# Performance work log

Hardware: AMD Instinct MI355X
Metric: run time of the kernel (lower is better)

## Reference

```python
import jax, jax.numpy as jnp
import numpy as np

B, N, M, K = 2, 50000, 50000, 16
C_IN, C_ADD, C_MID = 64, 3, 16


def setup_inputs() -> dict:
    key = jax.random.key(0)
    k1, k2, k3, k4 = jax.random.split(key, 4)
    return {
        "input_features": jax.random.normal(k1, (B, N, C_IN), dtype=jnp.float32),
        "neighbor_inds": jax.random.randint(k2, (B, M, K), 0, N, dtype=jnp.int64),
        "weightnet": jax.random.normal(k3, (B, M, K, C_MID), dtype=jnp.float32),
        "additional_features": jax.random.normal(k4, (B, M, K, C_ADD), dtype=jnp.float32),
    }


def reference(input_features, neighbor_inds, weightnet, additional_features):
    # Gather neighbor features: [B, M, K, C_in]
    gathered = jax.vmap(lambda feat, idx: feat[idx])(input_features, neighbor_inds)
    # Concatenate additional per-neighbor features: [B, M, K, C_in + C_add]
    cat = jnp.concatenate([gathered, additional_features], axis=-1)
    # Weighted reduce over neighbors: [B, M, C_total, C_mid]
    out = jnp.einsum("bmkc,bmkw->bmcw", cat, weightnet)
    b, m = out.shape[:2]
    return out.reshape(b, m, -1)
```

## Files before the change

kernel.cpp:

```cpp
#include <hip/hip_runtime.h>
#include <cstdint>
#include <cstddef>


namespace {
constexpr int B_   = 2;
constexpr int N_   = 50000;
constexpr int M_   = 50000;
constexpr int KNB  = 16;
constexpr int CIN  = 64;
constexpr int COUT = 67 * 16;
constexpr int PAIRS = B_ * M_;
constexpr int FELEMS = B_ * N_ * CIN;
}

typedef unsigned int u32;
typedef float  f32x4  __attribute__((ext_vector_type(4)));
typedef short  short8 __attribute__((ext_vector_type(8)));
typedef u32    u32x4  __attribute__((ext_vector_type(4)));
typedef u32    u32x2  __attribute__((ext_vector_type(2)));

struct IdxS   { int v[16]; };
struct StageT { unsigned short bg[4][8]; float ad[8]; float wf[8]; };
struct StageF { float bg[4][8]; float ad[8]; float wf[8]; };

static __device__ __forceinline__ short8 pack_bf8(const float* x) {
  u32x4 w;
  #pragma unroll
  for (int q = 0; q < 4; ++q)
    w[q] = __builtin_amdgcn_perm(__builtin_bit_cast(u32, x[2*q+1]),
                                 __builtin_bit_cast(u32, x[2*q]),
                                 0x07060302u);
  return __builtin_bit_cast(short8, w);
}

static __device__ __forceinline__ u32 bfrne(float x) {
  u32 u = __builtin_bit_cast(u32, x);
  return (u + 0x7FFFu + ((u >> 16) & 1u)) >> 16;
}

__global__ __launch_bounds__(256)
void cvt_feat_bf16(const float* __restrict__ src, unsigned short* __restrict__ dst) {
  const int n4 = FELEMS / 4;
  int i = blockIdx.x * blockDim.x + threadIdx.x;
  const int stride = gridDim.x * blockDim.x;
  const f32x4* s4 = reinterpret_cast<const f32x4*>(src);
  for (; i < n4; i += stride) {
    f32x4 v = s4[i];
    u32x2 w;
    w[0] = bfrne(v[0]) | (bfrne(v[1]) << 16);
    w[1] = bfrne(v[2]) | (bfrne(v[3]) << 16);
    *reinterpret_cast<u32x2*>(dst + 4 * (size_t)i) = w;
  }
}

static __device__ __forceinline__ void load_idx(const int* __restrict__ idxp, IdxS& r) {
  #pragma unroll
  for (int j = 0; j < 16; ++j)
    r.v[j] = __builtin_amdgcn_readfirstlane(idxp[j]);
}

static __device__ __forceinline__ void load_stage_t(const unsigned short* __restrict__ fb,
                                                    const float* __restrict__ wnp,
                                                    const float* __restrict__ adp,
                                                    const IdxS& I, int lane, StageT& S) {
  const int cc = lane & 15;
  if (lane < 32) {
    const int hi = lane >> 4;
    int rows[8];
    #pragma unroll
    for (int j = 0; j < 8; ++j) rows[j] = hi ? I.v[j + 8] : I.v[j];
    #pragma unroll
    for (int j = 0; j < 8; ++j) {
      const u32 rb = ((u32)rows[j]) << 6;
      #pragma unroll
      for (int t = 0; t < 4; ++t)
        S.bg[t][j] = fb[rb + (u32)(t * 16 + cc)];
    }
    const u32 woff = (hi ? 128u : 0u) + (u32)cc;
    #pragma unroll
    for (int j = 0; j < 8; ++j)
      S.wf[j] = __builtin_nontemporal_load(wnp + woff + j * 16);
    if (cc < 3) {
      const u32 aoff = (hi ? 24u : 0u) + (u32)cc;
      #pragma unroll
      for (int j = 0; j < 8; ++j)
        S.ad[j] = __builtin_nontemporal_load(adp + aoff + j * 3);
    }
  }
}

static __device__ __forceinline__ void compute_store_t(const StageT& S,
                                                       float* __restrict__ op, int lane) {
  const int cc = lane & 15, g = lane >> 4;
  const int soff = cc * 16 + g * 4;
  const short8 a = pack_bf8(S.wf);
  #pragma unroll
  for (int t = 0; t < 4; ++t) {
    short8 b;
    #pragma unroll
    for (int j = 0; j < 8; ++j) b[j] = (short)S.bg[t][j];
    f32x4 acc = {0.f, 0.f, 0.f, 0.f};
    acc = __builtin_amdgcn_mfma_f32_16x16x32_bf16(a, b, acc, 0, 0, 0);
    __builtin_nontemporal_store(acc, reinterpret_cast<f32x4*>(op + soff + t * 256));
  }
  {
    const short8 b = pack_bf8(S.ad);
    f32x4 acc = {0.f, 0.f, 0.f, 0.f};
    acc = __builtin_amdgcn_mfma_f32_16x16x32_bf16(a, b, acc, 0, 0, 0);
    if (cc < 3)
      __builtin_nontemporal_store(acc, reinterpret_cast<f32x4*>(op + soff + 1024));
  }
}

__global__ __launch_bounds__(256, 3)
void pconv6_tbl(const unsigned short* __restrict__ tbl, const int* __restrict__ inds,
                const float* __restrict__ wnet, const float* __restrict__ addf,
                float* __restrict__ out)
{
  const int lane = threadIdx.x & 63;
  const int gw = __builtin_amdgcn_readfirstlane(
      (int)((blockIdx.x * blockDim.x + threadIdx.x) >> 6));
  const int nw = (int)((gridDim.x * blockDim.x) >> 6);
  if (gw >= PAIRS) return;

  StageT sA = {}, sB = {};
  IdxS iA, iB;

  int p = gw;
  load_idx(inds + (size_t)p * KNB, iA);
  { const int p1 = (p + nw < PAIRS) ? (p + nw) : gw;
    load_idx(inds + (size_t)p1 * KNB, iB); }
  { const int b = p / M_;
    load_stage_t(tbl + (size_t)b * N_ * CIN, wnet + (size_t)p * 256,
                 addf + (size_t)p * 48, iA, lane, sA); }

  while (true) {
    {
      const int pf = (p + 2 * nw < PAIRS) ? (p + 2 * nw) : gw;
      load_idx(inds + (size_t)pf * KNB, iA);
      const int pn = (p + nw < PAIRS) ? (p + nw) : gw;
      const int bn = pn / M_;
      load_stage_t(tbl + (size_t)bn * N_ * CIN, wnet + (size_t)pn * 256,
                   addf + (size_t)pn * 48, iB, lane, sB);
      compute_store_t(sA, out + (size_t)p * COUT, lane);
    }
    p += nw; if (p >= PAIRS) break;
    {
      const int pf = (p + 2 * nw < PAIRS) ? (p + 2 * nw) : gw;
      load_idx(inds + (size_t)pf * KNB, iB);
      const int pn = (p + nw < PAIRS) ? (p + nw) : gw;
      const int bn = pn / M_;
      load_stage_t(tbl + (size_t)bn * N_ * CIN, wnet + (size_t)pn * 256,
                   addf + (size_t)pn * 48, iA, lane, sA);
      compute_store_t(sB, out + (size_t)p * COUT, lane);
    }
    p += nw; if (p >= PAIRS) break;
  }
}

static __device__ __forceinline__ void load_stage_f(const float* __restrict__ fb,
                                                    const float* __restrict__ wnp,
                                                    const float* __restrict__ adp,
                                                    const IdxS& I, int lane, StageF& S) {
  const int cc = lane & 15;
  if (lane < 32) {
    const int hi = lane >> 4;
    int rows[8];
    #pragma unroll
    for (int j = 0; j < 8; ++j) rows[j] = hi ? I.v[j + 8] : I.v[j];
    #pragma unroll
    for (int j = 0; j < 8; ++j) {
      const u32 rb = ((u32)rows[j]) << 6;
      #pragma unroll
      for (int t = 0; t < 4; ++t)
        S.bg[t][j] = fb[rb + (u32)(t * 16 + cc)];
    }
    const u32 woff = (hi ? 128u : 0u) + (u32)cc;
    #pragma unroll
    for (int j = 0; j < 8; ++j)
      S.wf[j] = __builtin_nontemporal_load(wnp + woff + j * 16);
    if (cc < 3) {
      const u32 aoff = (hi ? 24u : 0u) + (u32)cc;
      #pragma unroll
      for (int j = 0; j < 8; ++j)
        S.ad[j] = __builtin_nontemporal_load(adp + aoff + j * 3);
    }
  }
}

static __device__ __forceinline__ void compute_store_f(const StageF& S,
                                                       float* __restrict__ op, int lane) {
  const int cc = lane & 15, g = lane >> 4;
  const int soff = cc * 16 + g * 4;
  const short8 a = pack_bf8(S.wf);
  #pragma unroll
  for (int t = 0; t < 4; ++t) {
    const short8 b = pack_bf8(S.bg[t]);
    f32x4 acc = {0.f, 0.f, 0.f, 0.f};
    acc = __builtin_amdgcn_mfma_f32_16x16x32_bf16(a, b, acc, 0, 0, 0);
    __builtin_nontemporal_store(acc, reinterpret_cast<f32x4*>(op + soff + t * 256));
  }
  {
    const short8 b = pack_bf8(S.ad);
    f32x4 acc = {0.f, 0.f, 0.f, 0.f};
    acc = __builtin_amdgcn_mfma_f32_16x16x32_bf16(a, b, acc, 0, 0, 0);
    if (cc < 3)
      __builtin_nontemporal_store(acc, reinterpret_cast<f32x4*>(op + soff + 1024));
  }
}

__global__ __launch_bounds__(256, 3)
void pconv6_f32(const float* __restrict__ feat, const int* __restrict__ inds,
                const float* __restrict__ wnet, const float* __restrict__ addf,
                float* __restrict__ out)
{
  const int lane = threadIdx.x & 63;
  const int gw = __builtin_amdgcn_readfirstlane(
      (int)((blockIdx.x * blockDim.x + threadIdx.x) >> 6));
  const int nw = (int)((gridDim.x * blockDim.x) >> 6);
  if (gw >= PAIRS) return;

  StageF sA = {}, sB = {};
  IdxS iA, iB;

  int p = gw;
  load_idx(inds + (size_t)p * KNB, iA);
  { const int p1 = (p + nw < PAIRS) ? (p + nw) : gw;
    load_idx(inds + (size_t)p1 * KNB, iB); }
  { const int b = p / M_;
    load_stage_f(feat + (size_t)b * N_ * CIN, wnet + (size_t)p * 256,
                 addf + (size_t)p * 48, iA, lane, sA); }

  while (true) {
    {
      const int pf = (p + 2 * nw < PAIRS) ? (p + 2 * nw) : gw;
      load_idx(inds + (size_t)pf * KNB, iA);
      const int pn = (p + nw < PAIRS) ? (p + nw) : gw;
      const int bn = pn / M_;
      load_stage_f(feat + (size_t)bn * N_ * CIN, wnet + (size_t)pn * 256,
                   addf + (size_t)pn * 48, iB, lane, sB);
      compute_store_f(sA, out + (size_t)p * COUT, lane);
    }
    p += nw; if (p >= PAIRS) break;
    {
      const int pf = (p + 2 * nw < PAIRS) ? (p + 2 * nw) : gw;
      load_idx(inds + (size_t)pf * KNB, iB);
      const int pn = (p + nw < PAIRS) ? (p + nw) : gw;
      const int bn = pn / M_;
      load_stage_f(feat + (size_t)bn * N_ * CIN, wnet + (size_t)pn * 256,
                   addf + (size_t)pn * 48, iA, lane, sA);
      compute_store_f(sB, out + (size_t)p * COUT, lane);
    }
    p += nw; if (p >= PAIRS) break;
  }
}

extern "C" void kernel_launch(void* const* d_in, const int* in_sizes, int n_in,
                              void* d_out, int out_size, void* d_ws, size_t ws_size,
                              hipStream_t stream) {
  const float* feat = (const float*)d_in[0];
  const int*   inds = (const int*)d_in[1];
  const float* wnet = (const float*)d_in[2];
  const float* addf = (const float*)d_in[3];
  float* outp = (float*)d_out;

  const size_t TBL_BYTES = (size_t)FELEMS * sizeof(unsigned short);

  dim3 grid(2500), block(256);
  if (ws_size >= TBL_BYTES) {
    unsigned short* tbl = (unsigned short*)d_ws;
    hipLaunchKernelGGL(cvt_feat_bf16, dim3(2048), dim3(256), 0, stream, feat, tbl);
    hipLaunchKernelGGL(pconv6_tbl, grid, block, 0, stream,
                       tbl, inds, wnet, addf, outp);
  } else {
    hipLaunchKernelGGL(pconv6_f32, grid, block, 0, stream,
                       feat, inds, wnet, addf, outp);
  }
}
```

Before: 167.4 us.

## Replace double-buffered stage pipeline with single-stage loop at higher occupancy

Drops the two-deep software pipeline, which held two staged gather buffers in registers per wave. Each iteration now loads and computes one stage, and only the next pair's indices are prefetched. Launch bounds go from 3 to 4 waves and the grid from 2500 to 4096 blocks, so latency hiding comes from more resident waves instead of explicit overlap. The risk is that gather latency is exposed within each wave if the extra occupancy does not cover it.

```diff
diff --git a/kernel.cpp b/kernel.cpp
--- a/kernel.cpp
+++ b/kernel.cpp
@@ -113,8 +113,8 @@
   }
 }
 
-__global__ __launch_bounds__(256, 3)
-void pconv6_tbl(const unsigned short* __restrict__ tbl, const int* __restrict__ inds,
+__global__ __launch_bounds__(256, 4)
+void pconv7_tbl(const unsigned short* __restrict__ tbl, const int* __restrict__ inds,
                 const float* __restrict__ wnet, const float* __restrict__ addf,
                 float* __restrict__ out)
 {
@@ -124,38 +124,19 @@
   const int nw = (int)((gridDim.x * blockDim.x) >> 6);
   if (gw >= PAIRS) return;
 
-  StageT sA = {}, sB = {};
-  IdxS iA, iB;
-
-  int p = gw;
-  load_idx(inds + (size_t)p * KNB, iA);
-  { const int p1 = (p + nw < PAIRS) ? (p + nw) : gw;
-    load_idx(inds + (size_t)p1 * KNB, iB); }
-  { const int b = p / M_;
+  IdxS iCur, iNext;
+  load_idx(inds + (size_t)gw * KNB, iCur);
+
+  for (int p = gw; p < PAIRS; p += nw) {
+    const int pn = (p + nw < PAIRS) ? (p + nw) : gw;
+    load_idx(inds + (size_t)pn * KNB, iNext);
+    const int b = p / M_;
+    StageT S = {};
     load_stage_t(tbl + (size_t)b * N_ * CIN, wnet + (size_t)p * 256,
-                 addf + (size_t)p * 48, iA, lane, sA); }
-
-  while (true) {
-    {
-      const int pf = (p + 2 * nw < PAIRS) ? (p + 2 * nw) : gw;
-      load_idx(inds + (size_t)pf * KNB, iA);
-      const int pn = (p + nw < PAIRS) ? (p + nw) : gw;
-      const int bn = pn / M_;
-      load_stage_t(tbl + (size_t)bn * N_ * CIN, wnet + (size_t)pn * 256,
-                   addf + (size_t)pn * 48, iB, lane, sB);
-      compute_store_t(sA, out + (size_t)p * COUT, lane);
-    }
-    p += nw; if (p >= PAIRS) break;
-    {
-      const int pf = (p + 2 * nw < PAIRS) ? (p + 2 * nw) : gw;
-      load_idx(inds + (size_t)pf * KNB, iB);
-      const int pn = (p + nw < PAIRS) ? (p + nw) : gw;
-      const int bn = pn / M_;
-      load_stage_t(tbl + (size_t)bn * N_ * CIN, wnet + (size_t)pn * 256,
-                   addf + (size_t)pn * 48, iA, lane, sA);
-      compute_store_t(sB, out + (size_t)p * COUT, lane);
-    }
-    p += nw; if (p >= PAIRS) break;
+                 addf + (size_t)p * 48, iCur, lane, S);
+    compute_store_t(S, out + (size_t)p * COUT, lane);
+    #pragma unroll
+    for (int j = 0; j < 16; ++j) iCur.v[j] = iNext.v[j];
   }
 }
 
@@ -210,8 +191,8 @@
   }
 }
 
-__global__ __launch_bounds__(256, 3)
-void pconv6_f32(const float* __restrict__ feat, const int* __restrict__ inds,
+__global__ __launch_bounds__(256, 4)
+void pconv7_f32(const float* __restrict__ feat, const int* __restrict__ inds,
                 const float* __restrict__ wnet, const float* __restrict__ addf,
                 float* __restrict__ out)
 {
@@ -221,38 +202,19 @@
   const int nw = (int)((gridDim.x * blockDim.x) >> 6);
   if (gw >= PAIRS) return;
 
-  StageF sA = {}, sB = {};
-  IdxS iA, iB;
-
-  int p = gw;
-  load_idx(inds + (size_t)p * KNB, iA);
-  { const int p1 = (p + nw < PAIRS) ? (p + nw) : gw;
-    load_idx(inds + (size_t)p1 * KNB, iB); }
-  { const int b = p / M_;
+  IdxS iCur, iNext;
+  load_idx(inds + (size_t)gw * KNB, iCur);
+
+  for (int p = gw; p < PAIRS; p += nw) {
+    const int pn = (p + nw < PAIRS) ? (p + nw) : gw;
+    load_idx(inds + (size_t)pn * KNB, iNext);
+    const int b = p / M_;
+    StageF S = {};
     load_stage_f(feat + (size_t)b * N_ * CIN, wnet + (size_t)p * 256,
-                 addf + (size_t)p * 48, iA, lane, sA); }
-
-  while (true) {
-    {
-      const int pf = (p + 2 * nw < PAIRS) ? (p + 2 * nw) : gw;
-      load_idx(inds + (size_t)pf * KNB, iA);
-      const int pn = (p + nw < PAIRS) ? (p + nw) : gw;
-      const int bn = pn / M_;
-      load_stage_f(feat + (size_t)bn * N_ * CIN, wnet + (size_t)pn * 256,
-                   addf + (size_t)pn * 48, iB, lane, sB);
-      compute_store_f(sA, out + (size_t)p * COUT, lane);
-    }
-    p += nw; if (p >= PAIRS) break;
-    {
-      const int pf = (p + 2 * nw < PAIRS) ? (p + 2 * nw) : gw;
-      load_idx(inds + (size_t)pf * KNB, iB);
-      const int pn = (p + nw < PAIRS) ? (p + nw) : gw;
-      const int bn = pn / M_;
-      load_stage_f(feat + (size_t)bn * N_ * CIN, wnet + (size_t)pn * 256,
-                   addf + (size_t)pn * 48, iA, lane, sA);
-      compute_store_f(sB, out + (size_t)p * COUT, lane);
-    }
-    p += nw; if (p >= PAIRS) break;
+                 addf + (size_t)p * 48, iCur, lane, S);
+    compute_store_f(S, out + (size_t)p * COUT, lane);
+    #pragma unroll
+    for (int j = 0; j < 16; ++j) iCur.v[j] = iNext.v[j];
   }
 }
 
@@ -267,14 +229,14 @@
 
   const size_t TBL_BYTES = (size_t)FELEMS * sizeof(unsigned short);
 
-  dim3 grid(2500), block(256);
+  dim3 grid(4096), block(256);
   if (ws_size >= TBL_BYTES) {
     unsigned short* tbl = (unsigned short*)d_ws;
     hipLaunchKernelGGL(cvt_feat_bf16, dim3(2048), dim3(256), 0, stream, feat, tbl);
-    hipLaunchKernelGGL(pconv6_tbl, grid, block, 0, stream,
+    hipLaunchKernelGGL(pconv7_tbl, grid, block, 0, stream,
                        tbl, inds, wnet, addf, outp);
   } else {
-    hipLaunchKernelGGL(pconv6_f32, grid, block, 0, stream,
+    hipLaunchKernelGGL(pconv7_f32, grid, block, 0, stream,
                        feat, inds, wnet, addf, outp);
   }
 }
```

After: 162.6 us. 1.03x faster.
